# Kernel optimization log

Hardware: AMD Instinct MI355X
Metric: run time of the kernel (lower is better)

The kernel has to match this reference:

```python
import jax, jax.numpy as jnp
import numpy as np

B, N, DIN, DOUT, T, R, H = 4, 384, 128, 128, 4, 4, 8
DK = DOUT // H
SQRT_DK = float(np.sqrt(DK))


def setup_inputs() -> dict:
    key = jax.random.key(0)
    k = jax.random.split(key, 12)
    node_features = jax.random.normal(k[0], (B, N, DIN), jnp.float32)
    nt = jax.random.uniform(k[1], (B, N, T), dtype=jnp.float32)
    node_types_soft = nt / nt.sum(-1, keepdims=True)  # soft type distribution
    adj_matrix_soft = jax.random.uniform(k[2], (B, N, N), dtype=jnp.float32)
    et = jax.random.uniform(k[3], (B, N, N, R), dtype=jnp.float32)
    edge_types_soft = et / et.sum(-1, keepdims=True)  # soft relation distribution
    s = 0.05  # ~xavier scale for 128x128
    return dict(
        node_features=node_features,
        node_types_soft=node_types_soft,
        adj_matrix_soft=adj_matrix_soft,
        edge_types_soft=edge_types_soft,
        kw=jax.random.normal(k[4], (T, DIN, DOUT), jnp.float32) * s,
        kb=jnp.zeros((T, DOUT), jnp.float32),
        qw=jax.random.normal(k[5], (T, DIN, DOUT), jnp.float32) * s,
        qb=jnp.zeros((T, DOUT), jnp.float32),
        vw=jax.random.normal(k[6], (T, DIN, DOUT), jnp.float32) * s,
        vb=jnp.zeros((T, DOUT), jnp.float32),
        aw=jax.random.normal(k[7], (T, DOUT, DOUT), jnp.float32) * s,
        ab=jnp.zeros((T, DOUT), jnp.float32),
        norm_w=jnp.ones((T, DOUT), jnp.float32),
        norm_b=jnp.zeros((T, DOUT), jnp.float32),
        rel_pri=jnp.ones((R, H), jnp.float32),
        rel_att=jax.random.normal(k[8], (R, H, DK, DK), jnp.float32) * 0.1,
        rel_msg=jax.random.normal(k[9], (R, H, DK, DK), jnp.float32) * 0.1,
        skip=jnp.ones((T,), jnp.float32),
    )


def _forward(node_features, node_types_soft, adj_matrix_soft, edge_types_soft,
             kw, kb, qw, qb, vw, vb, aw, ab, norm_w, norm_b,
             rel_pri, rel_att, rel_msg, skip):
    Bq, Nn, _ = node_features.shape
    nt = node_types_soft
    # per-type Q/K/V projections: [B,N,T,H,DK]
    q = (jnp.einsum('bni,tid->bntd', node_features, qw) + qb).reshape(Bq, Nn, T, H, DK)
    kk = (jnp.einsum('bni,tid->bntd', node_features, kw) + kb).reshape(Bq, Nn, T, H, DK)
    v = (jnp.einsum('bni,tid->bntd', node_features, vw) + vb).reshape(Bq, Nn, T, H, DK)

    res_att = jnp.zeros((Bq, Nn, Nn, H), node_features.dtype)
    res_msg = jnp.zeros((Bq, Nn, Nn, H, DK), node_features.dtype)
    for r in range(R):  # small fixed relation count; types/heads fully vectorized
        kr = jnp.einsum('bjshe,hed->bjshd', kk, rel_att[r])
        vr = jnp.einsum('bjshe,hed->bjshd', v, rel_msg[r])
        # fold target-type mask (applied at node j in the original) into k: [B,N,Tt,Ts,H,DK]
        krt = kr[:, :, None] * nt[:, :, :, None, None, None]
        # P[b,i,j,s,h] = sum_{t,d} q[b,i,t,h,d] * nt[b,j,t] * kr[b,j,s,h,d], scaled
        P = jnp.einsum('bithd,bjtshd->bijsh', q, krt) * (rel_pri[r] / SQRT_DK)
        mask = edge_types_soft[..., r] * adj_matrix_soft  # [B,N,N]
        res_att = res_att + jnp.einsum('bijsh,bis->bijh', P, nt) * mask[..., None]
        res_msg = res_msg + jnp.einsum('bijsh,bis,bjshd->bijhd', P, nt, vr) * mask[..., None, None]

    att_sum = res_att.sum(axis=1, keepdims=True)
    safe = jnp.where(att_sum > 1e-6, att_sum, jnp.ones_like(att_sum))
    attw = (res_att / safe) * (att_sum > 1e-6).astype(res_att.dtype)
    agg = jnp.einsum('btsh,btshd->bthd', attw, res_msg).reshape(Bq, Nn, DOUT)

    trans = jnp.einsum('bnd,tdo->bnto', agg, aw) + ab
    trans = jax.nn.gelu(trans, approximate=False)  # dropout = identity at eval
    alpha = jax.nn.sigmoid(skip)[None, None, :, None]
    # in_dim == out_dim -> identity skip projection
    res = trans * alpha + node_features[:, :, None, :] * (1.0 - alpha)
    mean = res.mean(-1, keepdims=True)
    var = res.var(-1, keepdims=True)
    res = (res - mean) / jnp.sqrt(var + 1e-5) * norm_w + norm_b
    return (res * nt[..., None]).sum(axis=2)  # [B,N,DOUT]


def reference(node_features, node_types_soft, adj_matrix_soft, edge_types_soft,
              kw, kb, qw, qb, vw, vb, aw, ab, norm_w, norm_b,
              rel_pri, rel_att, rel_msg, skip):
    return _forward(node_features, node_types_soft, adj_matrix_soft, edge_types_soft,
                    kw, kb, qw, qb, vw, vb, aw, ab, norm_w, norm_b,
                    rel_pri, rel_att, rel_msg, skip)
```

## Files before the change

### kernel.cpp

```cpp
#include <hip/hip_runtime.h>
#include <math.h>

#define Bq 4
#define Nn 384
#define NB 1536
#define TT 4
#define RR 4
#define HH 8
#define DKk 16

typedef __attribute__((ext_vector_type(8))) short short8;
typedef __attribute__((ext_vector_type(4))) float f32x4;

__device__ __forceinline__ unsigned short f2bf(float f) {
  unsigned u = __float_as_uint(f);
  u += 0x7FFFu + ((u >> 16) & 1u);
  return (unsigned short)(u >> 16);
}

__device__ __forceinline__ void ld16(const float* __restrict__ p, float* o) {
  const float4* p4 = reinterpret_cast<const float4*>(p);
  float4 a = p4[0], b = p4[1], c = p4[2], d = p4[3];
  o[0]=a.x; o[1]=a.y; o[2]=a.z; o[3]=a.w;
  o[4]=b.x; o[5]=b.y; o[6]=b.z; o[7]=b.w;
  o[8]=c.x; o[9]=c.y; o[10]=c.z; o[11]=c.w;
  o[12]=d.x; o[13]=d.y; o[14]=d.z; o[15]=d.w;
}

__device__ __forceinline__ void bar_lds() {
  asm volatile("s_waitcnt lgkmcnt(0)" ::: "memory");
  __builtin_amdgcn_s_barrier();
}


__global__ __launch_bounds__(256) void k1a_qkv(
    const float* __restrict__ nf,
    const float* __restrict__ qw, const float* __restrict__ qb,
    const float* __restrict__ kw, const float* __restrict__ kb,
    const float* __restrict__ vw, const float* __restrict__ vb,
    float* __restrict__ q_ws, float* __restrict__ kv_k, float* __restrict__ kv_v)
{
  __shared__ float A_s[32][72];
  __shared__ float W_s[32][132];
  int mt = blockIdx.x, t = blockIdx.y, z = blockIdx.z;
  const float* W    = (z == 0) ? qw : ((z == 1) ? kw : vw);
  const float* bias = (z == 0) ? qb : ((z == 1) ? kb : vb);
  int tid = threadIdx.x;
  int colq = (tid & 31)*4, n8 = (tid >> 5)*8;
  float acc[8][4];
#pragma unroll
  for (int u = 0; u < 8; ++u)
#pragma unroll
    for (int c = 0; c < 4; ++c) acc[u][c] = 0.f;

  for (int kc = 0; kc < 4; ++kc) {
    __syncthreads();
    {
      int kk = tid & 31, nb0 = tid >> 5;
#pragma unroll
      for (int u = 0; u < 8; ++u)
        A_s[kk][nb0 + u*8] = nf[(size_t)(mt*64 + nb0 + u*8)*128 + kc*32 + kk];
#pragma unroll
      for (int u = 0; u < 4; ++u) {
        int idx = u*256 + tid;
        int wk = idx >> 5, c4 = (idx & 31)*4;
        *(float4*)&W_s[wk][c4] = *(const float4*)&W[(size_t)(t*128 + kc*32 + wk)*128 + c4];
      }
    }
    __syncthreads();
#pragma unroll
    for (int k = 0; k < 32; ++k) {
      float4 w4 = *(float4*)&W_s[k][colq];
      float a0[8];
      *(float4*)&a0[0] = *(float4*)&A_s[k][n8];
      *(float4*)&a0[4] = *(float4*)&A_s[k][n8 + 4];
#pragma unroll
      for (int u = 0; u < 8; ++u) {
        acc[u][0] += a0[u]*w4.x; acc[u][1] += a0[u]*w4.y;
        acc[u][2] += a0[u]*w4.z; acc[u][3] += a0[u]*w4.w;
      }
    }
  }
  float4 bv = *(const float4*)&bias[t*128 + colq];
#pragma unroll
  for (int u = 0; u < 8; ++u) {
    int node = mt*64 + n8 + u;
    float4 o;
    o.x = acc[u][0] + bv.x; o.y = acc[u][1] + bv.y;
    o.z = acc[u][2] + bv.z; o.w = acc[u][3] + bv.w;
    if (z == 0) {
      int h = colq >> 4, d = colq & 15;
      *(float4*)&q_ws[((size_t)h*NB + node)*64 + t*16 + d] = o;
    } else {
      float* dst = (z == 1) ? kv_k : kv_v;
      *(float4*)&dst[(size_t)node*512 + t*128 + colq] = o;
    }
  }
}

__global__ __launch_bounds__(256) void k1b_rel(
    const float* __restrict__ kv_k, const float* __restrict__ kv_v,
    const float* __restrict__ rel_att, const float* __restrict__ rel_msg,
    float* __restrict__ kr_ws, float* __restrict__ vr_ws)
{
  __shared__ float ra_s[4][16][16];
  __shared__ float rm_s[4][16][16];
  __shared__ float k_s[16][4][17];
  __shared__ float v_s[16][4][17];
  int nb = blockIdx.x, h = blockIdx.y;
  int n0 = nb*16;
  int tid = threadIdx.x;
#pragma unroll
  for (int u0 = 0; u0 < 4; ++u0) {
    int u = u0*256 + tid;
    int r = u >> 8, e = (u >> 4) & 15, d = u & 15;
    ra_s[r][e][d] = rel_att[((size_t)(r*8 + h)*16 + e)*16 + d];
    rm_s[r][e][d] = rel_msg[((size_t)(r*8 + h)*16 + e)*16 + d];
    int nl = u >> 6, s = (u >> 4) & 3, e2 = u & 15;
    k_s[nl][s][e2] = kv_k[(size_t)(n0 + nl)*512 + s*128 + h*16 + e2];
    v_s[nl][s][e2] = kv_v[(size_t)(n0 + nl)*512 + s*128 + h*16 + e2];
  }
  __syncthreads();
  int nl = tid >> 4, dq = tid & 15;
  size_t obase = ((size_t)h*NB + n0 + nl)*256;
#pragma unroll
  for (int r = 0; r < 4; ++r)
#pragma unroll
    for (int s = 0; s < 4; ++s) {
      float aK = 0.f, aV = 0.f;
#pragma unroll
      for (int e = 0; e < 16; ++e) {
        aK += k_s[nl][s][e] * ra_s[r][e][dq];
        aV += v_s[nl][s][e] * rm_s[r][e][dq];
      }
      kr_ws[obase + r*64 + s*16 + dq] = aK;
      vr_ws[obase + r*64 + s*16 + dq] = aV;
    }
}

__global__ __launch_bounds__(256,2) void k2_att(
    const float* __restrict__ nt, const float* __restrict__ adj,
    const float* __restrict__ ets, const float* __restrict__ rel_pri,
    const float* __restrict__ q_ws, const float* __restrict__ kr_ws,
    float* __restrict__ res_att, float* __restrict__ att_part)
{
  __shared__ float q_s[16*68];
  __shared__ float kr_s[32*260];
  __shared__ float ntj_s[32*4];
  __shared__ float nti_s[16*4];
  int it = blockIdx.x, h = blockIdx.y, b = blockIdx.z;
  int i0 = it*16;
  int tid = threadIdx.x;
  int j_l = tid>>3, ig = (tid>>1)&3, dh = tid&1;
  {
    int i = tid>>4, f = (tid&15)*4;
    float4 qv = *(const float4*)&q_ws[((size_t)(h*NB) + b*Nn + i0 + i)*64 + f];
    *(float4*)&q_s[i*68 + f] = qv;
  }
  if (tid < 64) nti_s[tid] = nt[(size_t)(b*Nn + i0 + (tid>>2))*TT + (tid&3)];
  float crr[4];
#pragma unroll
  for (int r = 0; r < 4; ++r) crr[r] = rel_pri[r*HH+h]*0.25f;

  for (int jc = 0; jc < 12; ++jc) {
    __syncthreads();
    {
      int js = tid>>3, gb = tid&7;
      const float* src = &kr_ws[((size_t)(h*NB) + b*Nn + jc*32 + js)*256];
      float* dst = &kr_s[js*260];
#pragma unroll
      for (int gl = 0; gl < 8; ++gl) {
        int g = gl*8 + gb;
        float4 v = *(const float4*)&src[g*4];
        int r = g>>4, s = (g>>2)&3, qd = g&3;
        int gd = (qd>>1)*32 + r*8 + s*2 + (qd&1);
        *(float4*)&dst[gd*4] = v;
      }
      if (tid < 128) ntj_s[tid] = nt[(size_t)(b*Nn + jc*32 + (tid>>2))*TT + (tid&3)];
    }
    __syncthreads();
    int j = jc*32 + j_l;
    float nt0 = ntj_s[j_l*4+0], nt1 = ntj_s[j_l*4+1];
    float nt2 = ntj_s[j_l*4+2], nt3 = ntj_s[j_l*4+3];
    float qn[4][8];
#pragma unroll
    for (int il = 0; il < 4; ++il) {
      int ib = (ig*4 + il)*68 + dh*8;
#pragma unroll
      for (int dp = 0; dp < 8; ++dp)
        qn[il][dp] = q_s[ib+dp]*nt0 + q_s[ib+16+dp]*nt1 + q_s[ib+32+dp]*nt2 + q_s[ib+48+dp]*nt3;
    }
    float mar[4][4];
#pragma unroll
    for (int il = 0; il < 4; ++il) {
      int i = i0 + ig*4 + il;
      float a = adj[((size_t)b*Nn + i)*Nn + j];
      float4 e4 = *(const float4*)&ets[(((size_t)b*Nn + i)*Nn + j)*RR];
      mar[il][0]=e4.x*a; mar[il][1]=e4.y*a; mar[il][2]=e4.z*a; mar[il][3]=e4.w*a;
    }
    float acc[4] = {0.f,0.f,0.f,0.f};
    const float* kbp = &kr_s[j_l*260 + dh*128];
#pragma unroll
    for (int r = 0; r < 4; ++r) {
      float mr0 = mar[0][r]*crr[r], mr1 = mar[1][r]*crr[r];
      float mr2 = mar[2][r]*crr[r], mr3 = mar[3][r]*crr[r];
#pragma unroll
      for (int s = 0; s < 4; ++s) {
        float kk[8];
        *(float4*)&kk[0] = *(const float4*)&kbp[r*32 + s*8];
        *(float4*)&kk[4] = *(const float4*)&kbp[r*32 + s*8 + 4];
        float d0=0,d1=0,d2=0,d3=0;
#pragma unroll
        for (int dp = 0; dp < 8; ++dp) {
          d0 += qn[0][dp]*kk[dp]; d1 += qn[1][dp]*kk[dp];
          d2 += qn[2][dp]*kk[dp]; d3 += qn[3][dp]*kk[dp];
        }
        d0 += __shfl_xor(d0,1); d1 += __shfl_xor(d1,1);
        d2 += __shfl_xor(d2,1); d3 += __shfl_xor(d3,1);
        acc[0] += mr0*nti_s[(ig*4+0)*4+s]*d0;
        acc[1] += mr1*nti_s[(ig*4+1)*4+s]*d1;
        acc[2] += mr2*nti_s[(ig*4+2)*4+s]*d2;
        acc[3] += mr3*nti_s[(ig*4+3)*4+s]*d3;
      }
    }
    if (dh == 0) {
#pragma unroll
      for (int il = 0; il < 4; ++il)
        res_att[((size_t)(b*HH + h)*Nn + i0 + ig*4 + il)*Nn + j] = acc[il];
    }
    float v = acc[0] + acc[1] + acc[2] + acc[3];
    v += __shfl_xor(v, 2);
    v += __shfl_xor(v, 4);
    if ((tid & 7) == 0)
      att_part[(size_t)it*12288 + (size_t)(b*HH + h)*Nn + j] = v;
  }
}

__global__ __launch_bounds__(256) void kb_inv(
    const float* __restrict__ att_part, float* __restrict__ att_inv)
{
  int idx = blockIdx.x*256 + threadIdx.x;
  float s = 0.f;
#pragma unroll
  for (int p = 0; p < 24; ++p) s += att_part[(size_t)p*12288 + idx];
  att_inv[idx] = (s > 1e-6f) ? 1.f/s : 0.f;
}

__global__ __launch_bounds__(256) void kc_agg(
    const float* __restrict__ nt, const float* __restrict__ adj,
    const float* __restrict__ ets, const float* __restrict__ rel_pri,
    const float* __restrict__ q_ws, const float* __restrict__ kr_ws,
    const float* __restrict__ vr_ws, const float* __restrict__ res_att,
    const float* __restrict__ att_inv, float* __restrict__ agg)
{
  __shared__ __align__(16) unsigned short B_lds[4][64*72];
  __shared__ __align__(16) unsigned short vr_lds[64*72];
  __shared__ __align__(16) unsigned short Z_lds[4][16*72];
  __shared__ float ntj_s[256];
  int it = blockIdx.x, jc = blockIdx.y, bh = blockIdx.z;
  int b = bh >> 3, h = bh & 7;
  int tid = threadIdx.x, w = tid >> 6, l = tid & 63;
  int j0 = jc*64;
  int ib = it*64 + w*16;
  int irow = ib + (l & 15);
  int iz = ib + ((l >> 4) << 2);
  int lq = (l >> 4) * 8;
  ntj_s[tid] = nt[(size_t)(b*Nn + j0 + (tid>>2))*4 + (tid&3)];
  short8 af[4][2];
  {
    float q0[8], q1[8];
    const float* qp = &q_ws[((size_t)h*NB + b*Nn + irow)*64];
    *(float4*)&q0[0] = *(const float4*)&qp[lq];
    *(float4*)&q0[4] = *(const float4*)&qp[lq + 4];
    *(float4*)&q1[0] = *(const float4*)&qp[32 + lq];
    *(float4*)&q1[4] = *(const float4*)&qp[32 + lq + 4];
    float4 ntiv = *(const float4*)&nt[(size_t)(b*Nn + irow)*4];
    float nta[4] = {ntiv.x, ntiv.y, ntiv.z, ntiv.w};
#pragma unroll
    for (int s = 0; s < 4; ++s)
#pragma unroll
      for (int e = 0; e < 8; ++e) {
        af[s][0][e] = (short)f2bf(q0[e]*nta[s]);
        af[s][1][e] = (short)f2bf(q1[e]*nta[s]);
      }
  }
  float crv[4];
#pragma unroll
  for (int r = 0; r < 4; ++r) crv[r] = rel_pri[r*HH + h]*0.25f;
  float cw[4][4];
  int eo[4][4];
  const float* ebase = ets + (size_t)b*Nn*Nn*4;
#pragma unroll
  for (int tj = 0; tj < 4; ++tj) {
    int j = j0 + tj*16 + (l & 15);
    float inv = att_inv[(size_t)bh*Nn + j];
#pragma unroll
    for (int p = 0; p < 4; ++p) {
      int i = iz + p;
      cw[tj][p] = res_att[((size_t)bh*Nn + i)*Nn + j] * inv
                * adj[((size_t)b*Nn + i)*Nn + j];
      eo[tj][p] = (i*Nn + j)*4;
    }
  }
  f32x4 agg_acc = {0.f,0.f,0.f,0.f};
  int js = tid >> 2, ss = tid & 3;
  const float* krp = &kr_ws[((size_t)h*NB + b*Nn + j0 + js)*256 + ss*16];
  const float* vrp = &vr_ws[((size_t)h*NB + b*Nn + j0 + js)*256 + ss*16];
  float kvA[16], vvA[16];
  ld16(krp, kvA);
  ld16(vrp, vvA);
  bar_lds();

#pragma unroll
  for (int r = 0; r < 4; ++r) {
    if (r) bar_lds();
    {
      float crr = crv[r];
      float4 ntjv = *(const float4*)&ntj_s[js*4];
      float nta[4] = {ntjv.x*crr, ntjv.y*crr, ntjv.z*crr, ntjv.w*crr};
#pragma unroll
      for (int t = 0; t < 4; ++t) {
#pragma unroll
        for (int dq = 0; dq < 2; ++dq) {
          short8 v;
#pragma unroll
          for (int e = 0; e < 8; ++e) v[e] = (short)f2bf(kvA[dq*8 + e]*nta[t]);
          *(short8*)&B_lds[ss][js*72 + t*16 + dq*8] = v;
        }
      }
#pragma unroll
      for (int d = 0; d < 16; ++d)
        vr_lds[(ss*16 + d)*72 + js] = f2bf(vvA[d]);
    }
    float kvB[16], vvB[16];
    if (r < 3) {
      ld16(krp + (r+1)*64, kvB);
      ld16(vrp + (r+1)*64, vvB);
    }
    bar_lds();
    float coef[4][4];
#pragma unroll
    for (int tj = 0; tj < 4; ++tj)
#pragma unroll
      for (int p = 0; p < 4; ++p)
        coef[tj][p] = ebase[eo[tj][p] + r] * cw[tj][p];
#pragma unroll
    for (int s = 0; s < 4; ++s) {
      f32x4 wacc[4];
#pragma unroll
      for (int tj = 0; tj < 4; ++tj) wacc[tj] = (f32x4){0.f,0.f,0.f,0.f};
#pragma unroll
      for (int tj = 0; tj < 4; ++tj) {
        short8 b0 = *(const short8*)&B_lds[s][(tj*16 + (l & 15))*72 + lq];
        short8 b1 = *(const short8*)&B_lds[s][(tj*16 + (l & 15))*72 + 32 + lq];
        wacc[tj] = __builtin_amdgcn_mfma_f32_16x16x32_bf16(af[s][0], b0, wacc[tj], 0, 0, 0);
        wacc[tj] = __builtin_amdgcn_mfma_f32_16x16x32_bf16(af[s][1], b1, wacc[tj], 0, 0, 0);
      }
#pragma unroll
      for (int tj = 0; tj < 4; ++tj)
#pragma unroll
        for (int p = 0; p < 4; ++p)
          Z_lds[w][(((l >> 4)*4) + p)*72 + tj*16 + (l & 15)] = f2bf(wacc[tj][p]*coef[tj][p]);
#pragma unroll
      for (int kj = 0; kj < 2; ++kj) {
        short8 zf = *(const short8*)&Z_lds[w][(l & 15)*72 + kj*32 + lq];
        short8 vf = *(const short8*)&vr_lds[(s*16 + (l & 15))*72 + kj*32 + lq];
        agg_acc = __builtin_amdgcn_mfma_f32_16x16x32_bf16(zf, vf, agg_acc, 0, 0, 0);
      }
    }
    if (r < 3) {
#pragma unroll
      for (int e = 0; e < 16; ++e) { kvA[e] = kvB[e]; vvA[e] = vvB[e]; }
    }
  }
#pragma unroll
  for (int p = 0; p < 4; ++p)
    atomicAdd(&agg[((size_t)b*Nn + iz + p)*128 + h*16 + (l & 15)], agg_acc[p]);
}

__global__ __launch_bounds__(128) void k5_out(
    const float* __restrict__ agg_ws, const float* __restrict__ nf,
    const float* __restrict__ nt, const float* __restrict__ aw,
    const float* __restrict__ ab, const float* __restrict__ norm_w,
    const float* __restrict__ norm_b, const float* __restrict__ skip,
    float* __restrict__ out)
{
  __shared__ float agg_s[128];
  __shared__ float red[4];
  int n = blockIdx.x, b = blockIdx.y;
  int o = threadIdx.x;
  size_t node = (size_t)b*Nn + n;
  agg_s[o] = agg_ws[node*128 + o];
  __syncthreads();
  float nfo = nf[node*128 + o];
  float outacc = 0.f;
  for (int t = 0; t < TT; ++t) {
    float a = ab[t*128 + o];
    for (int dd = 0; dd < 128; ++dd) a += agg_s[dd] * aw[(size_t)(t*128 + dd)*128 + o];
    float g = 0.5f * a * (1.f + erff(a * 0.70710678118654752f));
    float alpha = 1.f / (1.f + expf(-skip[t]));
    float res = g*alpha + nfo*(1.f - alpha);
    float s1 = res, s2 = res*res;
#pragma unroll
    for (int m = 32; m >= 1; m >>= 1) { s1 += __shfl_xor(s1, m); s2 += __shfl_xor(s2, m); }
    int w = o >> 6;
    if ((o & 63) == 0) { red[w*2] = s1; red[w*2 + 1] = s2; }
    __syncthreads();
    float tot1 = red[0] + red[2], tot2 = red[1] + red[3];
    __syncthreads();
    float mean = tot1 * (1.f/128.f);
    float var  = tot2 * (1.f/128.f) - mean*mean;
    float nrm = (res - mean) * rsqrtf(var + 1e-5f) * norm_w[t*128 + o] + norm_b[t*128 + o];
    outacc += nrm * nt[node*TT + t];
  }
  out[node*128 + o] = outacc;
}

extern "C" void kernel_launch(void* const* d_in, const int* in_sizes, int n_in,
                              void* d_out, int out_size, void* d_ws, size_t ws_size,
                              hipStream_t stream) {
  const float* nf      = (const float*)d_in[0];
  const float* nts     = (const float*)d_in[1];
  const float* adj     = (const float*)d_in[2];
  const float* ets     = (const float*)d_in[3];
  const float* kw      = (const float*)d_in[4];
  const float* kb      = (const float*)d_in[5];
  const float* qw      = (const float*)d_in[6];
  const float* qb      = (const float*)d_in[7];
  const float* vw      = (const float*)d_in[8];
  const float* vb      = (const float*)d_in[9];
  const float* aw      = (const float*)d_in[10];
  const float* ab      = (const float*)d_in[11];
  const float* normw   = (const float*)d_in[12];
  const float* normb   = (const float*)d_in[13];
  const float* rel_pri = (const float*)d_in[14];
  const float* rel_att = (const float*)d_in[15];
  const float* rel_msg = (const float*)d_in[16];
  const float* skip    = (const float*)d_in[17];
  (void)in_sizes; (void)n_in; (void)out_size; (void)ws_size;

  float* ws = (float*)d_ws;
  float* q_ws    = ws;
  float* kr_ws   = q_ws + 786432;
  float* vr_ws   = kr_ws + 3145728;
  float* res_att = vr_ws + 3145728;
  float* att_part= res_att + 4718592;
  float* att_inv = att_part + 294912;
  float* agg_ws  = att_inv + 12288;
  float* kv_k = res_att;
  float* kv_v = res_att + 786432;

  hipMemsetAsync(agg_ws, 0, (size_t)196608*4, stream);
  hipLaunchKernelGGL(k1a_qkv, dim3(24, 4, 3), dim3(256), 0, stream,
                     nf, qw, qb, kw, kb, vw, vb, q_ws, kv_k, kv_v);
  hipLaunchKernelGGL(k1b_rel, dim3(96, 8), dim3(256), 0, stream,
                     kv_k, kv_v, rel_att, rel_msg, kr_ws, vr_ws);
  hipLaunchKernelGGL(k2_att, dim3(24, 8, 4), dim3(256), 0, stream,
                     nts, adj, ets, rel_pri, q_ws, kr_ws, res_att, att_part);
  hipLaunchKernelGGL(kb_inv, dim3(48), dim3(256), 0, stream, att_part, att_inv);
  hipLaunchKernelGGL(kc_agg, dim3(6, 6, 32), dim3(256), 0, stream,
                     nts, adj, ets, rel_pri, q_ws, kr_ws, vr_ws, res_att, att_inv, agg_ws);
  hipLaunchKernelGGL(k5_out, dim3(384, 4), dim3(128), 0, stream,
                     agg_ws, nf, nts, aw, ab, normw, normb, skip, (float*)d_out);
}
```

Baseline: 204.3 us.

## Fold memset and inverse-sum kernel into neighbors, split attention grid over j halves

Zeroing of the aggregation buffer moves into k1b_rel, so the separate memset is gone. The kb_inv reduction kernel is removed: kc_agg now sums the 24 partial column sums itself and computes the inverse in shared memory. k2_att doubles its grid by splitting the j loop into two halves, for more blocks and better occupancy. Together these remove two launches and raise parallelism, at the cost of every kc_agg block redundantly reducing the partial sums.

```diff
diff --git a/kernel.cpp b/kernel.cpp
--- a/kernel.cpp
+++ b/kernel.cpp
@@ -8,6 +8,7 @@
 #define RR 4
 #define HH 8
 #define DKk 16
+#define APART 12288
 
 typedef __attribute__((ext_vector_type(8))) short short8;
 typedef __attribute__((ext_vector_type(4))) float f32x4;
@@ -101,7 +102,8 @@
 __global__ __launch_bounds__(256) void k1b_rel(
     const float* __restrict__ kv_k, const float* __restrict__ kv_v,
     const float* __restrict__ rel_att, const float* __restrict__ rel_msg,
-    float* __restrict__ kr_ws, float* __restrict__ vr_ws)
+    float* __restrict__ kr_ws, float* __restrict__ vr_ws,
+    float* __restrict__ agg)
 {
   __shared__ float ra_s[4][16][16];
   __shared__ float rm_s[4][16][16];
@@ -110,6 +112,7 @@
   int nb = blockIdx.x, h = blockIdx.y;
   int n0 = nb*16;
   int tid = threadIdx.x;
+  agg[(size_t)(n0 + (tid >> 4))*128 + h*16 + (tid & 15)] = 0.f;
 #pragma unroll
   for (int u0 = 0; u0 < 4; ++u0) {
     int u = u0*256 + tid;
@@ -148,7 +151,8 @@
   __shared__ float kr_s[32*260];
   __shared__ float ntj_s[32*4];
   __shared__ float nti_s[16*4];
-  int it = blockIdx.x, h = blockIdx.y, b = blockIdx.z;
+  int bx = blockIdx.x, h = blockIdx.y, b = blockIdx.z;
+  int it = bx >> 1, jh = bx & 1;
   int i0 = it*16;
   int tid = threadIdx.x;
   int j_l = tid>>3, ig = (tid>>1)&3, dh = tid&1;
@@ -162,7 +166,7 @@
 #pragma unroll
   for (int r = 0; r < 4; ++r) crr[r] = rel_pri[r*HH+h]*0.25f;
 
-  for (int jc = 0; jc < 12; ++jc) {
+  for (int jc = jh*6; jc < jh*6 + 6; ++jc) {
     __syncthreads();
     {
       int js = tid>>3, gb = tid&7;
@@ -232,18 +236,8 @@
     v += __shfl_xor(v, 2);
     v += __shfl_xor(v, 4);
     if ((tid & 7) == 0)
-      att_part[(size_t)it*12288 + (size_t)(b*HH + h)*Nn + j] = v;
-  }
-}
-
-__global__ __launch_bounds__(256) void kb_inv(
-    const float* __restrict__ att_part, float* __restrict__ att_inv)
-{
-  int idx = blockIdx.x*256 + threadIdx.x;
-  float s = 0.f;
-#pragma unroll
-  for (int p = 0; p < 24; ++p) s += att_part[(size_t)p*12288 + idx];
-  att_inv[idx] = (s > 1e-6f) ? 1.f/s : 0.f;
+      att_part[(size_t)it*APART + (size_t)(b*HH + h)*Nn + j] = v;
+  }
 }
 
 __global__ __launch_bounds__(256) void kc_agg(
@@ -251,12 +245,13 @@
     const float* __restrict__ ets, const float* __restrict__ rel_pri,
     const float* __restrict__ q_ws, const float* __restrict__ kr_ws,
     const float* __restrict__ vr_ws, const float* __restrict__ res_att,
-    const float* __restrict__ att_inv, float* __restrict__ agg)
+    const float* __restrict__ att_part, float* __restrict__ agg)
 {
   __shared__ __align__(16) unsigned short B_lds[4][64*72];
   __shared__ __align__(16) unsigned short vr_lds[64*72];
   __shared__ __align__(16) unsigned short Z_lds[4][16*72];
   __shared__ float ntj_s[256];
+  __shared__ float inv_s[64];
   int it = blockIdx.x, jc = blockIdx.y, bh = blockIdx.z;
   int b = bh >> 3, h = bh & 7;
   int tid = threadIdx.x, w = tid >> 6, l = tid & 63;
@@ -266,6 +261,13 @@
   int iz = ib + ((l >> 4) << 2);
   int lq = (l >> 4) * 8;
   ntj_s[tid] = nt[(size_t)(b*Nn + j0 + (tid>>2))*4 + (tid&3)];
+  if (tid < 64) {
+    float s = 0.f;
+#pragma unroll
+    for (int p = 0; p < 24; ++p)
+      s += att_part[(size_t)p*APART + (size_t)bh*Nn + j0 + tid];
+    inv_s[tid] = (s > 1e-6f) ? 1.f/s : 0.f;
+  }
   short8 af[4][2];
   {
     float q0[8], q1[8];
@@ -293,11 +295,10 @@
 #pragma unroll
   for (int tj = 0; tj < 4; ++tj) {
     int j = j0 + tj*16 + (l & 15);
-    float inv = att_inv[(size_t)bh*Nn + j];
 #pragma unroll
     for (int p = 0; p < 4; ++p) {
       int i = iz + p;
-      cw[tj][p] = res_att[((size_t)bh*Nn + i)*Nn + j] * inv
+      cw[tj][p] = res_att[((size_t)bh*Nn + i)*Nn + j]
                 * adj[((size_t)b*Nn + i)*Nn + j];
       eo[tj][p] = (i*Nn + j)*4;
     }
@@ -310,6 +311,12 @@
   ld16(krp, kvA);
   ld16(vrp, vvA);
   bar_lds();
+#pragma unroll
+  for (int tj = 0; tj < 4; ++tj) {
+    float inv = inv_s[tj*16 + (l & 15)];
+#pragma unroll
+    for (int p = 0; p < 4; ++p) cw[tj][p] *= inv;
+  }
 
 #pragma unroll
   for (int r = 0; r < 4; ++r) {
@@ -445,21 +452,18 @@
   float* vr_ws   = kr_ws + 3145728;
   float* res_att = vr_ws + 3145728;
   float* att_part= res_att + 4718592;
-  float* att_inv = att_part + 294912;
-  float* agg_ws  = att_inv + 12288;
+  float* agg_ws  = att_part + 294912 + 12288;
   float* kv_k = res_att;
   float* kv_v = res_att + 786432;
 
-  hipMemsetAsync(agg_ws, 0, (size_t)196608*4, stream);
   hipLaunchKernelGGL(k1a_qkv, dim3(24, 4, 3), dim3(256), 0, stream,
                      nf, qw, qb, kw, kb, vw, vb, q_ws, kv_k, kv_v);
   hipLaunchKernelGGL(k1b_rel, dim3(96, 8), dim3(256), 0, stream,
-                     kv_k, kv_v, rel_att, rel_msg, kr_ws, vr_ws);
-  hipLaunchKernelGGL(k2_att, dim3(24, 8, 4), dim3(256), 0, stream,
+                     kv_k, kv_v, rel_att, rel_msg, kr_ws, vr_ws, agg_ws);
+  hipLaunchKernelGGL(k2_att, dim3(48, 8, 4), dim3(256), 0, stream,
                      nts, adj, ets, rel_pri, q_ws, kr_ws, res_att, att_part);
-  hipLaunchKernelGGL(kb_inv, dim3(48), dim3(256), 0, stream, att_part, att_inv);
   hipLaunchKernelGGL(kc_agg, dim3(6, 6, 32), dim3(256), 0, stream,
-                     nts, adj, ets, rel_pri, q_ws, kr_ws, vr_ws, res_att, att_inv, agg_ws);
+                     nts, adj, ets, rel_pri, q_ws, kr_ws, vr_ws, res_att, att_part, agg_ws);
   hipLaunchKernelGGL(k5_out, dim3(384, 4), dim3(128), 0, stream,
                      agg_ws, nf, nts, aw, ab, normw, normb, skip, (float*)d_out);
 }
```

Result: faster. 194.6 us (-4.7%).
